# Kernel optimization log

Measured on AMD Instinct MI355X. Metric: run time of the kernel, lower is better.

## Reference

```python
import jax, jax.numpy as jnp
import numpy as np

B, S, D, HD = 4, 4096, 1024, 64

def setup_inputs() -> dict:
    key = jax.random.key(0)
    ks = jax.random.split(key, 4)
    scale = 1.0 / np.sqrt(D)
    return {
        "x": jax.random.normal(ks[0], (B, S, D), dtype=jnp.float32),
        "wq": jax.random.normal(ks[1], (HD, D), dtype=jnp.float32) * scale,
        "bq": jnp.zeros((HD,), dtype=jnp.float32),
        "wk": jax.random.normal(ks[2], (HD, D), dtype=jnp.float32) * scale,
        "bk": jnp.zeros((HD,), dtype=jnp.float32),
        "wv": jax.random.normal(ks[3], (HD, D), dtype=jnp.float32) * scale,
        "bv": jnp.zeros((HD,), dtype=jnp.float32),
    }

def reference(x, wq, bq, wk, bk, wv, bv):
    seq_len = x.shape[1]
    head_dim = wq.shape[0]
    # projections: nn.Linear stores weight as [out, in]
    q = jnp.einsum('bsd,hd->bsh', x, wq) + bq  # [B,S,HD]
    k = jnp.einsum('bsd,hd->bsh', x, wk) + bk
    v = jnp.einsum('bsd,hd->bsh', x, wv) + bv
    score = jnp.einsum('bqh,bkh->bqk', q, k) / jnp.sqrt(jnp.float32(head_dim))  # [B,S,S]
    causal = jnp.tril(jnp.ones((seq_len, seq_len), dtype=bool))
    score = jnp.where(causal, score, -jnp.inf)
    attn = jax.nn.softmax(score, axis=-1)
    # dropout p=0.0 -> identity
    out = jnp.einsum('bqk,bkh->bqh', attn, v)  # [B,S,HD]
    return out
```

## Files before the change

kernel.cpp:

```cpp
#include <hip/hip_runtime.h>
#include <math.h>

#define B_   4
#define S_   4096
#define D_   1024
#define HD_  64

#define CK            8
#define CHUNKS_PER_B  288
#define PSTRIDE       68
#define SLOT_F        (64 * PSTRIDE)

typedef float  f32x4  __attribute__((ext_vector_type(4)));
typedef __bf16 bf16x8 __attribute__((ext_vector_type(8)));

static __device__ __forceinline__ unsigned short f2bf(float f) {
    unsigned int u = __float_as_uint(f);
    u += 0x7FFFu + ((u >> 16) & 1u);
    return (unsigned short)(u >> 16);
}

__global__ __launch_bounds__(256) void convert_w(
    const float* __restrict__ wq, const float* __restrict__ wk,
    const float* __restrict__ wv, unsigned short* __restrict__ wbf)
{
    const int col = blockIdx.x;
    const int p = col >> 6, h = col & 63;
    const float* src = (p == 0 ? wq : (p == 1 ? wk : wv)) + (size_t)h * D_;
    const int t = threadIdx.x;
    const float4 v = ((const float4*)src)[t];
    ushort4 o;
    o.x = f2bf(v.x); o.y = f2bf(v.y); o.z = f2bf(v.z); o.w = f2bf(v.w);
    *(ushort4*)&wbf[(size_t)col * D_ + 4 * t] = o;
}

__global__ __launch_bounds__(256) void proj_mfma(
    const float* __restrict__ x, const unsigned short* __restrict__ wbf,
    const float* __restrict__ bq, const float* __restrict__ bk,
    const float* __restrict__ bv,
    unsigned short* __restrict__ qbf, unsigned short* __restrict__ kbf,
    unsigned short* __restrict__ vtb)
{
    __shared__ unsigned short xs[32][136];
    __shared__ unsigned short wsh[96][136];

    const int t = threadIdx.x;
    const int w = t >> 6, lane = t & 63;
    const int n = lane & 15, g = lane >> 4;
    const int koff = 8 * g;
    const int rt = w & 1, cg = w >> 1;
    const size_t row0 = (size_t)blockIdx.x * 32;
    const int colbase = 96 * blockIdx.y;

    f32x4 acc[3];
#pragma unroll
    for (int i = 0; i < 3; ++i) acc[i] = (f32x4)0.f;

    for (int chunk = 0; chunk < 8; ++chunk) {
        const int d0 = chunk * 128;
        __syncthreads();
#pragma unroll
        for (int i = 0; i < 4; ++i) {
            int e = t + i * 256;
            int r = e >> 5, c4 = (e & 31) * 4;
            float4 v = *(const float4*)&x[(row0 + r) * D_ + d0 + c4];
            ushort4 o;
            o.x = f2bf(v.x); o.y = f2bf(v.y); o.z = f2bf(v.z); o.w = f2bf(v.w);
            *(ushort4*)&xs[r][c4] = o;
        }
#pragma unroll
        for (int i = 0; i < 6; ++i) {
            int e = t + i * 256;
            int col = e >> 4, g8 = (e & 15) * 8;
            uint4 v = *(const uint4*)&wbf[(size_t)(colbase + col) * D_ + d0 + g8];
            *(uint4*)&wsh[col][g8] = v;
        }
        __syncthreads();

#pragma unroll
        for (int ks = 0; ks < 4; ++ks) {
            const int k0 = 32 * ks;
            const bf16x8 a = *(const bf16x8*)&xs[16 * rt + n][k0 + koff];
#pragma unroll
            for (int ci = 0; ci < 3; ++ci) {
                const bf16x8 b = *(const bf16x8*)&wsh[48 * cg + 16 * ci + n][k0 + koff];
                acc[ci] = __builtin_amdgcn_mfma_f32_16x16x32_bf16(a, b, acc[ci], 0, 0, 0);
            }
        }
    }

#pragma unroll
    for (int ci = 0; ci < 3; ++ci) {
        const int gct = 6 * blockIdx.y + 3 * cg + ci;
        const int p = gct >> 2, h0 = (gct & 3) * 16;
        const int h = h0 + n;
        const float bb = (p == 0 ? bq : (p == 1 ? bk : bv))[h];
        if (p == 2) {
            const size_t grow0 = row0 + 16 * rt + 4 * g;
            const int bidx = (int)(grow0 >> 12);
            const int s0 = (int)(grow0 & 4095);
            ushort4 u;
            u.x = f2bf(acc[ci][0] + bb); u.y = f2bf(acc[ci][1] + bb);
            u.z = f2bf(acc[ci][2] + bb); u.w = f2bf(acc[ci][3] + bb);
            *(ushort4*)&vtb[((size_t)bidx * HD_ + h) * S_ + s0] = u;
        } else {
            unsigned short* outp = (p == 0 ? qbf : kbf);
            const float scale = (p == 0) ? 0.125f : 1.0f;
#pragma unroll
            for (int r = 0; r < 4; ++r) {
                const size_t grow = row0 + 16 * rt + 4 * g + r;
                outp[grow * HD_ + h] = f2bf((acc[ci][r] + bb) * scale);
            }
        }
    }
}

__global__ __launch_bounds__(256) void flash_splitk(
    const unsigned short* __restrict__ qg, const unsigned short* __restrict__ kg,
    const unsigned short* __restrict__ vt, float* __restrict__ out,
    float* __restrict__ part)
{
    __shared__ unsigned short qsh[64][72];
    __shared__ unsigned short ksh[64][72];
    __shared__ unsigned short vsh[64][72];
    __shared__ unsigned short psh[4][16][72];

    const int t    = threadIdx.x;
    const int w    = t >> 6;
    const int lane = t & 63;
    const int n    = lane & 15;
    const int g    = lane >> 4;
    const int koff = 8 * g;
    const int b    = blockIdx.y;

    int qi = 0, rem = blockIdx.x;
    while (rem >= ((qi >> 3) + 1)) { rem -= (qi >> 3) + 1; ++qi; }
    const int c   = rem;
    const int kt0 = c * CK;
    const int kt1 = min(qi, kt0 + CK - 1);
    const int nc  = (qi >> 3) + 1;

    const size_t qtile = ((size_t)b * S_ + (size_t)qi * 64) * HD_;

    {
        const uint4* src = (const uint4*)(qg + qtile);
#pragma unroll
        for (int i = 0; i < 2; ++i) {
            int e = t + i * 256;
            int r = e >> 3, gg = e & 7;
            *(uint4*)&qsh[r][8 * gg] = src[e];
        }
    }

    f32x4 o4[4];
#pragma unroll
    for (int i = 0; i < 4; ++i) o4[i] = (f32x4)0.f;
    float m_r = -INFINITY, l_r = 0.f;

    for (int kt = kt0; kt <= kt1; ++kt) {
        const size_t kvbase = ((size_t)b * S_ + (size_t)kt * 64) * HD_;
        __syncthreads();
        {
            const uint4* ksrc = (const uint4*)(kg + kvbase);
#pragma unroll
            for (int i = 0; i < 2; ++i) {
                int e = t + i * 256;
                int r = e >> 3, gg = e & 7;
                *(uint4*)&ksh[r][8 * gg] = ksrc[e];
            }
#pragma unroll
            for (int i = 0; i < 2; ++i) {
                int e = t + i * 256;
                int h = e >> 3, gg = e & 7;
                *(uint4*)&vsh[h][8 * gg] =
                    *(const uint4*)&vt[((size_t)b * HD_ + h) * S_ + kt * 64 + 8 * gg];
            }
        }
        __syncthreads();

        f32x4 sc[4];
#pragma unroll
        for (int mt = 0; mt < 4; ++mt) sc[mt] = (f32x4)0.f;
#pragma unroll
        for (int ks = 0; ks < 2; ++ks) {
            const bf16x8 bq8 = *(const bf16x8*)&qsh[16 * w + n][32 * ks + koff];
#pragma unroll
            for (int mt = 0; mt < 4; ++mt) {
                const bf16x8 ak = *(const bf16x8*)&ksh[16 * mt + n][32 * ks + koff];
                sc[mt] = __builtin_amdgcn_mfma_f32_16x16x32_bf16(ak, bq8, sc[mt], 0, 0, 0);
            }
        }

        if (kt == qi) {
            const int qloc = 16 * w + n;
#pragma unroll
            for (int mt = 0; mt < 4; ++mt)
#pragma unroll
                for (int r = 0; r < 4; ++r) {
                    const int kloc = 16 * mt + 4 * g + r;
                    if (kloc > qloc) sc[mt][r] = -INFINITY;
                }
        }

        float mx = -INFINITY;
#pragma unroll
        for (int mt = 0; mt < 4; ++mt)
#pragma unroll
            for (int r = 0; r < 4; ++r) mx = fmaxf(mx, sc[mt][r]);
        mx = fmaxf(mx, __shfl_xor(mx, 16));
        mx = fmaxf(mx, __shfl_xor(mx, 32));

        const float m_new = fmaxf(m_r, mx);
        const float alpha = __expf(m_r - m_new);
        float psum = 0.f;
#pragma unroll
        for (int mt = 0; mt < 4; ++mt)
#pragma unroll
            for (int r = 0; r < 4; ++r) {
                const float p = __expf(sc[mt][r] - m_new);
                sc[mt][r] = p;
                psum += p;
            }
        psum += __shfl_xor(psum, 16);
        psum += __shfl_xor(psum, 32);
        l_r = l_r * alpha + psum;
        m_r = m_new;

#pragma unroll
        for (int r = 0; r < 4; ++r) {
            const float ar = __shfl(alpha, 4 * g + r);
#pragma unroll
            for (int ht = 0; ht < 4; ++ht) o4[ht][r] *= ar;
        }

#pragma unroll
        for (int mt = 0; mt < 4; ++mt) {
            ushort4 u;
            u.x = f2bf(sc[mt][0]); u.y = f2bf(sc[mt][1]);
            u.z = f2bf(sc[mt][2]); u.w = f2bf(sc[mt][3]);
            *(ushort4*)&psh[w][n][16 * mt + 4 * g] = u;
        }

#pragma unroll
        for (int ks = 0; ks < 2; ++ks) {
            const bf16x8 ap = *(const bf16x8*)&psh[w][n][32 * ks + koff];
#pragma unroll
            for (int ht = 0; ht < 4; ++ht) {
                const bf16x8 bv8 = *(const bf16x8*)&vsh[16 * ht + n][32 * ks + koff];
                o4[ht] = __builtin_amdgcn_mfma_f32_16x16x32_bf16(ap, bv8, o4[ht], 0, 0, 0);
            }
        }
    }

    const size_t qbase = ((size_t)b * S_ + (size_t)qi * 64) * HD_;
    if (nc == 1) {
#pragma unroll
        for (int r = 0; r < 4; ++r) {
            const float lr = __shfl(l_r, 4 * g + r);
            const float inv = 1.f / lr;
            const size_t ob = qbase + (size_t)(16 * w + 4 * g + r) * HD_;
#pragma unroll
            for (int ht = 0; ht < 4; ++ht)
                out[ob + 16 * ht + n] = o4[ht][r] * inv;
        }
    } else {
        const size_t sb = ((size_t)b * CHUNKS_PER_B + blockIdx.x) * SLOT_F;
#pragma unroll
        for (int r = 0; r < 4; ++r) {
            const size_t pb = sb + (size_t)(16 * w + 4 * g + r) * PSTRIDE;
#pragma unroll
            for (int ht = 0; ht < 4; ++ht)
                part[pb + 16 * ht + n] = o4[ht][r];
        }
        if (g == 0) {
            part[sb + (size_t)(16 * w + n) * PSTRIDE + 64] = m_r;
            part[sb + (size_t)(16 * w + n) * PSTRIDE + 65] = l_r;
        }
    }
}

__global__ __launch_bounds__(256) void combine(
    const float* __restrict__ part, float* __restrict__ out)
{
    const int t  = threadIdx.x;
    const int qr = t >> 2, tc = t & 3;
    const int qi = blockIdx.x + CK;
    const int b  = blockIdx.y;
    const int nc = (qi >> 3) + 1;

    int cum = 0;
    for (int j = 0; j < qi; ++j) cum += (j >> 3) + 1;
    const size_t base0 = ((size_t)b * CHUNKS_PER_B + cum) * SLOT_F;

    float M = -INFINITY;
    for (int c0 = 0; c0 < nc; ++c0)
        M = fmaxf(M, part[base0 + (size_t)c0 * SLOT_F + qr * PSTRIDE + 64]);

    float L = 0.f;
    float o[16];
#pragma unroll
    for (int j = 0; j < 16; ++j) o[j] = 0.f;

    for (int c0 = 0; c0 < nc; ++c0) {
        const size_t sb = base0 + (size_t)c0 * SLOT_F + qr * PSTRIDE;
        const float m_c = part[sb + 64];
        const float l_c = part[sb + 65];
        const float w = __expf(m_c - M);
        L += w * l_c;
#pragma unroll
        for (int j = 0; j < 4; ++j) {
            const float4 ov = *(const float4*)&part[sb + tc * 16 + 4 * j];
            o[4 * j + 0] += w * ov.x; o[4 * j + 1] += w * ov.y;
            o[4 * j + 2] += w * ov.z; o[4 * j + 3] += w * ov.w;
        }
    }

    const float inv = 1.f / L;
    const size_t qbase = ((size_t)b * S_ + (size_t)qi * 64) * HD_;
#pragma unroll
    for (int j = 0; j < 4; ++j) {
        float4 r;
        r.x = o[4 * j + 0] * inv; r.y = o[4 * j + 1] * inv;
        r.z = o[4 * j + 2] * inv; r.w = o[4 * j + 3] * inv;
        *(float4*)&out[qbase + 16 * t + 4 * j] = r;
    }
}

extern "C" void kernel_launch(void* const* d_in, const int* in_sizes, int n_in,
                              void* d_out, int out_size, void* d_ws, size_t ws_size,
                              hipStream_t stream)
{
    const float* x  = (const float*)d_in[0];
    const float* wq = (const float*)d_in[1];
    const float* bq = (const float*)d_in[2];
    const float* wk = (const float*)d_in[3];
    const float* bk = (const float*)d_in[4];
    const float* wv = (const float*)d_in[5];
    const float* bv = (const float*)d_in[6];
    float* outp = (float*)d_out;

    const size_t n = (size_t)B_ * S_ * HD_;
    unsigned short* qbf = (unsigned short*)d_ws;
    unsigned short* kbf = qbf + n;
    unsigned short* vtb = kbf + n;
    unsigned short* wbf = vtb + n;
    float* part = (float*)(wbf + (size_t)192 * D_);

    convert_w<<<dim3(192), 256, 0, stream>>>(wq, wk, wv, wbf);
    proj_mfma<<<dim3(B_ * S_ / 32, 2), 256, 0, stream>>>(
        x, wbf, bq, bk, bv, qbf, kbf, vtb);
    flash_splitk<<<dim3(CHUNKS_PER_B, B_), 256, 0, stream>>>(qbf, kbf, vtb, outp, part);
    combine<<<dim3(S_ / 64 - CK, B_), 256, 0, stream>>>(part, outp);
}
```

Baseline: 156.0 us.

## Process two adjacent query tiles per block to share K/V tile loads

Each flash block now handles a pair of consecutive 64-row query tiles with 512 threads (8 waves), so every K/V tile loaded into shared memory serves both tiles. The grid is halved, and each thread does a single K/V load per iteration. Partial-output slot indexing is recomputed per query tile so the existing combine kernel still works. In exchange there are fewer blocks, more LDS per block, and waves for the lower tile sit idle on the last diagonal key tile.

```diff
diff --git a/kernel.cpp b/kernel.cpp
--- a/kernel.cpp
+++ b/kernel.cpp
@@ -8,6 +8,7 @@
 
 #define CK            8
 #define CHUNKS_PER_B  288
+#define PAIRS_CHUNKS  144
 #define PSTRIDE       68
 #define SLOT_F        (64 * PSTRIDE)
 
@@ -115,15 +116,15 @@
     }
 }
 
-__global__ __launch_bounds__(256) void flash_splitk(
+__global__ __launch_bounds__(512) void flash_splitk(
     const unsigned short* __restrict__ qg, const unsigned short* __restrict__ kg,
     const unsigned short* __restrict__ vt, float* __restrict__ out,
     float* __restrict__ part)
 {
-    __shared__ unsigned short qsh[64][72];
+    __shared__ unsigned short qsh[128][72];
     __shared__ unsigned short ksh[64][72];
     __shared__ unsigned short vsh[64][72];
-    __shared__ unsigned short psh[4][16][72];
+    __shared__ unsigned short psh[8][16][72];
 
     const int t    = threadIdx.x;
     const int w    = t >> 6;
@@ -131,22 +132,24 @@
     const int n    = lane & 15;
     const int g    = lane >> 4;
     const int koff = 8 * g;
+    const int qt   = w >> 2;
+    const int wq   = w & 3;
     const int b    = blockIdx.y;
 
-    int qi = 0, rem = blockIdx.x;
-    while (rem >= ((qi >> 3) + 1)) { rem -= (qi >> 3) + 1; ++qi; }
-    const int c   = rem;
-    const int kt0 = c * CK;
-    const int kt1 = min(qi, kt0 + CK - 1);
-    const int nc  = (qi >> 3) + 1;
-
-    const size_t qtile = ((size_t)b * S_ + (size_t)qi * 64) * HD_;
+    int p = 0, rem = blockIdx.x;
+    while (rem >= (((2 * p + 1) >> 3) + 1)) { rem -= ((2 * p + 1) >> 3) + 1; ++p; }
+    const int c    = rem;
+    const int qiA  = 2 * p;
+    const int qi_w = qiA + qt;
+    const int kt0  = c * CK;
+    const int kt1  = min(qiA + 1, kt0 + CK - 1);
+    const int nc   = ((qiA + 1) >> 3) + 1;
 
     {
-        const uint4* src = (const uint4*)(qg + qtile);
+        const uint4* src = (const uint4*)(qg + ((size_t)b * S_ + (size_t)qiA * 64) * HD_);
 #pragma unroll
         for (int i = 0; i < 2; ++i) {
-            int e = t + i * 256;
+            int e = t + i * 512;
             int r = e >> 3, gg = e & 7;
             *(uint4*)&qsh[r][8 * gg] = src[e];
         }
@@ -156,125 +159,121 @@
 #pragma unroll
     for (int i = 0; i < 4; ++i) o4[i] = (f32x4)0.f;
     float m_r = -INFINITY, l_r = 0.f;
+
+    const int qrow = 64 * qt + 16 * wq;
 
     for (int kt = kt0; kt <= kt1; ++kt) {
         const size_t kvbase = ((size_t)b * S_ + (size_t)kt * 64) * HD_;
         __syncthreads();
         {
-            const uint4* ksrc = (const uint4*)(kg + kvbase);
-#pragma unroll
-            for (int i = 0; i < 2; ++i) {
-                int e = t + i * 256;
-                int r = e >> 3, gg = e & 7;
-                *(uint4*)&ksh[r][8 * gg] = ksrc[e];
-            }
-#pragma unroll
-            for (int i = 0; i < 2; ++i) {
-                int e = t + i * 256;
-                int h = e >> 3, gg = e & 7;
-                *(uint4*)&vsh[h][8 * gg] =
-                    *(const uint4*)&vt[((size_t)b * HD_ + h) * S_ + kt * 64 + 8 * gg];
-            }
+            const int r = t >> 3, gg = t & 7;
+            *(uint4*)&ksh[r][8 * gg] = *(const uint4*)&kg[kvbase + (size_t)r * HD_ + 8 * gg];
+            *(uint4*)&vsh[r][8 * gg] =
+                *(const uint4*)&vt[((size_t)b * HD_ + r) * S_ + kt * 64 + 8 * gg];
         }
         __syncthreads();
 
-        f32x4 sc[4];
-#pragma unroll
-        for (int mt = 0; mt < 4; ++mt) sc[mt] = (f32x4)0.f;
-#pragma unroll
-        for (int ks = 0; ks < 2; ++ks) {
-            const bf16x8 bq8 = *(const bf16x8*)&qsh[16 * w + n][32 * ks + koff];
+        if (kt <= qi_w) {
+            f32x4 sc[4];
+#pragma unroll
+            for (int mt = 0; mt < 4; ++mt) sc[mt] = (f32x4)0.f;
+#pragma unroll
+            for (int ks = 0; ks < 2; ++ks) {
+                const bf16x8 bq8 = *(const bf16x8*)&qsh[qrow + n][32 * ks + koff];
+#pragma unroll
+                for (int mt = 0; mt < 4; ++mt) {
+                    const bf16x8 ak = *(const bf16x8*)&ksh[16 * mt + n][32 * ks + koff];
+                    sc[mt] = __builtin_amdgcn_mfma_f32_16x16x32_bf16(ak, bq8, sc[mt], 0, 0, 0);
+                }
+            }
+
+            if (kt == qi_w) {
+                const int qloc = 16 * wq + n;
+#pragma unroll
+                for (int mt = 0; mt < 4; ++mt)
+#pragma unroll
+                    for (int r = 0; r < 4; ++r) {
+                        const int kloc = 16 * mt + 4 * g + r;
+                        if (kloc > qloc) sc[mt][r] = -INFINITY;
+                    }
+            }
+
+            float mx = -INFINITY;
+#pragma unroll
+            for (int mt = 0; mt < 4; ++mt)
+#pragma unroll
+                for (int r = 0; r < 4; ++r) mx = fmaxf(mx, sc[mt][r]);
+            mx = fmaxf(mx, __shfl_xor(mx, 16));
+            mx = fmaxf(mx, __shfl_xor(mx, 32));
+
+            const float m_new = fmaxf(m_r, mx);
+            const float alpha = __expf(m_r - m_new);
+            float psum = 0.f;
+#pragma unroll
+            for (int mt = 0; mt < 4; ++mt)
+#pragma unroll
+                for (int r = 0; r < 4; ++r) {
+                    const float pe = __expf(sc[mt][r] - m_new);
+                    sc[mt][r] = pe;
+                    psum += pe;
+                }
+            psum += __shfl_xor(psum, 16);
+            psum += __shfl_xor(psum, 32);
+            l_r = l_r * alpha + psum;
+            m_r = m_new;
+
+#pragma unroll
+            for (int r = 0; r < 4; ++r) {
+                const float ar = __shfl(alpha, 4 * g + r);
+#pragma unroll
+                for (int ht = 0; ht < 4; ++ht) o4[ht][r] *= ar;
+            }
+
 #pragma unroll
             for (int mt = 0; mt < 4; ++mt) {
-                const bf16x8 ak = *(const bf16x8*)&ksh[16 * mt + n][32 * ks + koff];
-                sc[mt] = __builtin_amdgcn_mfma_f32_16x16x32_bf16(ak, bq8, sc[mt], 0, 0, 0);
-            }
-        }
-
-        if (kt == qi) {
-            const int qloc = 16 * w + n;
-#pragma unroll
-            for (int mt = 0; mt < 4; ++mt)
-#pragma unroll
-                for (int r = 0; r < 4; ++r) {
-                    const int kloc = 16 * mt + 4 * g + r;
-                    if (kloc > qloc) sc[mt][r] = -INFINITY;
+                ushort4 u;
+                u.x = f2bf(sc[mt][0]); u.y = f2bf(sc[mt][1]);
+                u.z = f2bf(sc[mt][2]); u.w = f2bf(sc[mt][3]);
+                *(ushort4*)&psh[w][n][16 * mt + 4 * g] = u;
+            }
+
+#pragma unroll
+            for (int ks = 0; ks < 2; ++ks) {
+                const bf16x8 ap = *(const bf16x8*)&psh[w][n][32 * ks + koff];
+#pragma unroll
+                for (int ht = 0; ht < 4; ++ht) {
+                    const bf16x8 bv8 = *(const bf16x8*)&vsh[16 * ht + n][32 * ks + koff];
+                    o4[ht] = __builtin_amdgcn_mfma_f32_16x16x32_bf16(ap, bv8, o4[ht], 0, 0, 0);
                 }
-        }
-
-        float mx = -INFINITY;
-#pragma unroll
-        for (int mt = 0; mt < 4; ++mt)
-#pragma unroll
-            for (int r = 0; r < 4; ++r) mx = fmaxf(mx, sc[mt][r]);
-        mx = fmaxf(mx, __shfl_xor(mx, 16));
-        mx = fmaxf(mx, __shfl_xor(mx, 32));
-
-        const float m_new = fmaxf(m_r, mx);
-        const float alpha = __expf(m_r - m_new);
-        float psum = 0.f;
-#pragma unroll
-        for (int mt = 0; mt < 4; ++mt)
-#pragma unroll
-            for (int r = 0; r < 4; ++r) {
-                const float p = __expf(sc[mt][r] - m_new);
-                sc[mt][r] = p;
-                psum += p;
-            }
-        psum += __shfl_xor(psum, 16);
-        psum += __shfl_xor(psum, 32);
-        l_r = l_r * alpha + psum;
-        m_r = m_new;
-
-#pragma unroll
-        for (int r = 0; r < 4; ++r) {
-            const float ar = __shfl(alpha, 4 * g + r);
-#pragma unroll
-            for (int ht = 0; ht < 4; ++ht) o4[ht][r] *= ar;
-        }
-
-#pragma unroll
-        for (int mt = 0; mt < 4; ++mt) {
-            ushort4 u;
-            u.x = f2bf(sc[mt][0]); u.y = f2bf(sc[mt][1]);
-            u.z = f2bf(sc[mt][2]); u.w = f2bf(sc[mt][3]);
-            *(ushort4*)&psh[w][n][16 * mt + 4 * g] = u;
-        }
-
-#pragma unroll
-        for (int ks = 0; ks < 2; ++ks) {
-            const bf16x8 ap = *(const bf16x8*)&psh[w][n][32 * ks + koff];
-#pragma unroll
-            for (int ht = 0; ht < 4; ++ht) {
-                const bf16x8 bv8 = *(const bf16x8*)&vsh[16 * ht + n][32 * ks + koff];
-                o4[ht] = __builtin_amdgcn_mfma_f32_16x16x32_bf16(ap, bv8, o4[ht], 0, 0, 0);
-            }
-        }
-    }
-
-    const size_t qbase = ((size_t)b * S_ + (size_t)qi * 64) * HD_;
+            }
+        }
+    }
+
+    const size_t qbase = ((size_t)b * S_ + (size_t)qi_w * 64) * HD_;
     if (nc == 1) {
 #pragma unroll
         for (int r = 0; r < 4; ++r) {
             const float lr = __shfl(l_r, 4 * g + r);
             const float inv = 1.f / lr;
-            const size_t ob = qbase + (size_t)(16 * w + 4 * g + r) * HD_;
+            const size_t ob = qbase + (size_t)(16 * wq + 4 * g + r) * HD_;
 #pragma unroll
             for (int ht = 0; ht < 4; ++ht)
                 out[ob + 16 * ht + n] = o4[ht][r] * inv;
         }
     } else {
-        const size_t sb = ((size_t)b * CHUNKS_PER_B + blockIdx.x) * SLOT_F;
+        int cum = 0;
+        for (int j = 0; j < qi_w; ++j) cum += (j >> 3) + 1;
+        const size_t sb = ((size_t)b * CHUNKS_PER_B + cum + c) * SLOT_F;
 #pragma unroll
         for (int r = 0; r < 4; ++r) {
-            const size_t pb = sb + (size_t)(16 * w + 4 * g + r) * PSTRIDE;
+            const size_t pb = sb + (size_t)(16 * wq + 4 * g + r) * PSTRIDE;
 #pragma unroll
             for (int ht = 0; ht < 4; ++ht)
                 part[pb + 16 * ht + n] = o4[ht][r];
         }
         if (g == 0) {
-            part[sb + (size_t)(16 * w + n) * PSTRIDE + 64] = m_r;
-            part[sb + (size_t)(16 * w + n) * PSTRIDE + 65] = l_r;
+            part[sb + (size_t)(16 * wq + n) * PSTRIDE + 64] = m_r;
+            part[sb + (size_t)(16 * wq + n) * PSTRIDE + 65] = l_r;
         }
     }
 }
@@ -349,6 +348,6 @@
     convert_w<<<dim3(192), 256, 0, stream>>>(wq, wk, wv, wbf);
     proj_mfma<<<dim3(B_ * S_ / 32, 2), 256, 0, stream>>>(
         x, wbf, bq, bk, bv, qbf, kbf, vtb);
-    flash_splitk<<<dim3(CHUNKS_PER_B, B_), 256, 0, stream>>>(qbf, kbf, vtb, outp, part);
+    flash_splitk<<<dim3(PAIRS_CHUNKS, B_), 512, 0, stream>>>(qbf, kbf, vtb, outp, part);
     combine<<<dim3(S_ / 64 - CK, B_), 256, 0, stream>>>(part, outp);
 }
```

Result: slower. 160.7 us (+3.0%).

## Reorder flash split-K blocks full-chunks-first and transpose PV MFMA for vector stores

Applied to the files above, without the earlier changes.

Flattens the attention grid to one dimension. All full 8-tile chunks across batches are scheduled first and the partial (diagonal) chunks last, which should improve load balance and reduce the tail. The P·V MFMA operands are swapped so each lane holds four consecutive head-dim values of one query row. That removes the alpha and l shuffles and allows float4 stores to the output and partial buffers. A closed-form chunk_slot replaces the loop-based slot index in both kernels, and the changed register layout and slot mapping must stay consistent with combine.

```diff
diff --git a/kernel.cpp b/kernel.cpp
--- a/kernel.cpp
+++ b/kernel.cpp
@@ -8,6 +8,7 @@
 
 #define CK            8
 #define CHUNKS_PER_B  288
+#define FULL_CHUNKS   224
 #define PSTRIDE       68
 #define SLOT_F        (64 * PSTRIDE)
 
@@ -18,6 +19,11 @@
     unsigned int u = __float_as_uint(f);
     u += 0x7FFFu + ((u >> 16) & 1u);
     return (unsigned short)(u >> 16);
+}
+
+static __device__ __forceinline__ int chunk_slot(int qi, int c) {
+    const int a = qi >> 3, r = qi & 7;
+    return qi + 4 * a * (a - 1) + a * r + c;
 }
 
 __global__ __launch_bounds__(256) void convert_w(
@@ -131,11 +137,23 @@
     const int n    = lane & 15;
     const int g    = lane >> 4;
     const int koff = 8 * g;
-    const int b    = blockIdx.y;
-
-    int qi = 0, rem = blockIdx.x;
-    while (rem >= ((qi >> 3) + 1)) { rem -= (qi >> 3) + 1; ++qi; }
-    const int c   = rem;
+
+    int b, qi, c;
+    {
+        const int idx = blockIdx.x;
+        if (idx < B_ * FULL_CHUNKS) {
+            b = idx / FULL_CHUNKS;
+            int rem = idx - b * FULL_CHUNKS;
+            qi = 8;
+            while (rem >= (qi >> 3)) { rem -= (qi >> 3); ++qi; }
+            c = rem;
+        } else {
+            const int r2 = idx - B_ * FULL_CHUNKS;
+            b = r2 >> 6;
+            qi = r2 & 63;
+            c = qi >> 3;
+        }
+    }
     const int kt0 = c * CK;
     const int kt1 = min(qi, kt0 + CK - 1);
     const int nc  = (qi >> 3) + 1;
@@ -217,9 +235,9 @@
         for (int mt = 0; mt < 4; ++mt)
 #pragma unroll
             for (int r = 0; r < 4; ++r) {
-                const float p = __expf(sc[mt][r] - m_new);
-                sc[mt][r] = p;
-                psum += p;
+                const float pe = __expf(sc[mt][r] - m_new);
+                sc[mt][r] = pe;
+                psum += pe;
             }
         psum += __shfl_xor(psum, 16);
         psum += __shfl_xor(psum, 32);
@@ -227,11 +245,9 @@
         m_r = m_new;
 
 #pragma unroll
-        for (int r = 0; r < 4; ++r) {
-            const float ar = __shfl(alpha, 4 * g + r);
-#pragma unroll
-            for (int ht = 0; ht < 4; ++ht) o4[ht][r] *= ar;
-        }
+        for (int ht = 0; ht < 4; ++ht)
+#pragma unroll
+            for (int r = 0; r < 4; ++r) o4[ht][r] *= alpha;
 
 #pragma unroll
         for (int mt = 0; mt < 4; ++mt) {
@@ -246,35 +262,36 @@
             const bf16x8 ap = *(const bf16x8*)&psh[w][n][32 * ks + koff];
 #pragma unroll
             for (int ht = 0; ht < 4; ++ht) {
-                const bf16x8 bv8 = *(const bf16x8*)&vsh[16 * ht + n][32 * ks + koff];
-                o4[ht] = __builtin_amdgcn_mfma_f32_16x16x32_bf16(ap, bv8, o4[ht], 0, 0, 0);
+                const bf16x8 av = *(const bf16x8*)&vsh[16 * ht + n][32 * ks + koff];
+                o4[ht] = __builtin_amdgcn_mfma_f32_16x16x32_bf16(av, ap, o4[ht], 0, 0, 0);
             }
         }
     }
 
     const size_t qbase = ((size_t)b * S_ + (size_t)qi * 64) * HD_;
     if (nc == 1) {
-#pragma unroll
-        for (int r = 0; r < 4; ++r) {
-            const float lr = __shfl(l_r, 4 * g + r);
-            const float inv = 1.f / lr;
-            const size_t ob = qbase + (size_t)(16 * w + 4 * g + r) * HD_;
-#pragma unroll
-            for (int ht = 0; ht < 4; ++ht)
-                out[ob + 16 * ht + n] = o4[ht][r] * inv;
+        const float inv = 1.f / l_r;
+        const size_t ob = qbase + (size_t)(16 * w + n) * HD_;
+#pragma unroll
+        for (int ht = 0; ht < 4; ++ht) {
+            float4 rv;
+            rv.x = o4[ht][0] * inv; rv.y = o4[ht][1] * inv;
+            rv.z = o4[ht][2] * inv; rv.w = o4[ht][3] * inv;
+            *(float4*)&out[ob + 16 * ht + 4 * g] = rv;
         }
     } else {
-        const size_t sb = ((size_t)b * CHUNKS_PER_B + blockIdx.x) * SLOT_F;
-#pragma unroll
-        for (int r = 0; r < 4; ++r) {
-            const size_t pb = sb + (size_t)(16 * w + 4 * g + r) * PSTRIDE;
-#pragma unroll
-            for (int ht = 0; ht < 4; ++ht)
-                part[pb + 16 * ht + n] = o4[ht][r];
+        const size_t sb = ((size_t)b * CHUNKS_PER_B + chunk_slot(qi, c)) * SLOT_F;
+        const size_t pb = sb + (size_t)(16 * w + n) * PSTRIDE;
+#pragma unroll
+        for (int ht = 0; ht < 4; ++ht) {
+            float4 rv;
+            rv.x = o4[ht][0]; rv.y = o4[ht][1];
+            rv.z = o4[ht][2]; rv.w = o4[ht][3];
+            *(float4*)&part[pb + 16 * ht + 4 * g] = rv;
         }
         if (g == 0) {
-            part[sb + (size_t)(16 * w + n) * PSTRIDE + 64] = m_r;
-            part[sb + (size_t)(16 * w + n) * PSTRIDE + 65] = l_r;
+            part[pb + 64] = m_r;
+            part[pb + 65] = l_r;
         }
     }
 }
@@ -288,9 +305,7 @@
     const int b  = blockIdx.y;
     const int nc = (qi >> 3) + 1;
 
-    int cum = 0;
-    for (int j = 0; j < qi; ++j) cum += (j >> 3) + 1;
-    const size_t base0 = ((size_t)b * CHUNKS_PER_B + cum) * SLOT_F;
+    const size_t base0 = ((size_t)b * CHUNKS_PER_B + chunk_slot(qi, 0)) * SLOT_F;
 
     float M = -INFINITY;
     for (int c0 = 0; c0 < nc; ++c0)
@@ -349,6 +364,6 @@
     convert_w<<<dim3(192), 256, 0, stream>>>(wq, wk, wv, wbf);
     proj_mfma<<<dim3(B_ * S_ / 32, 2), 256, 0, stream>>>(
         x, wbf, bq, bk, bv, qbf, kbf, vtb);
-    flash_splitk<<<dim3(CHUNKS_PER_B, B_), 256, 0, stream>>>(qbf, kbf, vtb, outp, part);
+    flash_splitk<<<dim3(B_ * CHUNKS_PER_B), 256, 0, stream>>>(qbf, kbf, vtb, outp, part);
     combine<<<dim3(S_ / 64 - CK, B_), 256, 0, stream>>>(part, outp);
 }
```

Measured after the change: 154.9 us. About the same (-0.7%).
